# Optimization experiments

Hardware: AMD Instinct MI355X
Metric: run time of the kernel (lower is better)

The kernel has to match this reference:

```python
import jax, jax.numpy as jnp
import numpy as np

DIM = 512
HEADS = 8
DIM_HEAD = 64
INNER = HEADS * DIM_HEAD  # 512
EPS = 1e-5
SCALE = DIM_HEAD ** (-0.5)


def setup_inputs() -> dict:
    key = jax.random.key(0)
    ks = jax.random.split(key, 12)
    B, S = 8, 1024
    x = jax.random.normal(ks[0], (B, DIM, S, 1), dtype=jnp.float32)
    # BatchNorm2d params (eval mode: running stats)
    bn_gamma = jax.random.normal(ks[1], (DIM,), dtype=jnp.float32) * 0.1 + 1.0
    bn_beta = jax.random.normal(ks[2], (DIM,), dtype=jnp.float32) * 0.1
    bn_mean = jax.random.normal(ks[3], (DIM,), dtype=jnp.float32) * 0.1
    bn_var = jax.random.uniform(ks[4], (DIM,), dtype=jnp.float32, minval=0.5, maxval=1.5)
    # 1x1 Conv2d == linear: weight [out, in], bias [out]
    def lin(k, out_d, in_d):
        kw, kb = jax.random.split(k)
        lim = 1.0 / np.sqrt(in_d)
        w = jax.random.uniform(kw, (out_d, in_d), dtype=jnp.float32, minval=-lim, maxval=lim)
        b = jax.random.uniform(kb, (out_d,), dtype=jnp.float32, minval=-lim, maxval=lim)
        return w, b
    wq, bq = lin(ks[5], INNER, DIM)
    wk, bk = lin(ks[6], INNER, DIM)
    wv, bv = lin(ks[7], INNER, DIM)
    wo, bo = lin(ks[8], DIM, INNER)
    return {"x": x, "bn_gamma": bn_gamma, "bn_beta": bn_beta,
            "bn_mean": bn_mean, "bn_var": bn_var,
            "wq": wq, "bq": bq, "wk": wk, "bk": bk,
            "wv": wv, "bv": bv, "wo": wo, "bo": bo}


def reference(x, bn_gamma, bn_beta, bn_mean, bn_var,
              wq, bq, wk, bk, wv, bv, wo, bo):
    B, C, S, _ = x.shape
    # BatchNorm2d (eval) over channel dim
    inv = jax.lax.rsqrt(bn_var + EPS)
    xn = (x - bn_mean[None, :, None, None]) * (bn_gamma * inv)[None, :, None, None] \
         + bn_beta[None, :, None, None]
    t = jnp.transpose(xn[..., 0], (0, 2, 1))  # [B, S, C]
    q = (t @ wq.T + bq).reshape(B, S, HEADS, DIM_HEAD)
    k = (t @ wk.T + bk).reshape(B, S, HEADS, DIM_HEAD)
    v = (t @ wv.T + bv).reshape(B, S, HEADS, DIM_HEAD)
    scores = jnp.einsum('bshd,bthd->bhst', q, k) * SCALE  # [B,H,S,S]
    attn = jax.nn.softmax(scores, axis=-1)
    o = jnp.einsum('bhst,bthd->bshd', attn, v).reshape(B, S, INNER)
    y = o @ wo.T + bo  # [B, S, C]
    return jnp.transpose(y, (0, 2, 1))[..., None]  # [B, C, S, 1]
```

## Files before the change

kernel.cpp:

```cpp
#include <hip/hip_runtime.h>
#include <stdint.h>

typedef __bf16 bf16;
typedef bf16 bf16x8 __attribute__((ext_vector_type(8)));
typedef bf16 bf16x4 __attribute__((ext_vector_type(4)));
typedef float f32x4 __attribute__((ext_vector_type(4)));

#define NB 8
#define NS 1024
#define NC 512
#define NH 8
#define ND 64

#define QSCALE 0.18033688011f

__device__ __forceinline__ void gload16(const void* g, void* l) {
  __builtin_amdgcn_global_load_lds(
      (const __attribute__((address_space(1))) void*)g,
      (__attribute__((address_space(3))) void*)l, 16, 0, 0);
}

__global__ __launch_bounds__(256) void prep_kernel(
    const float* __restrict__ x, const float* __restrict__ gam,
    const float* __restrict__ bet, const float* __restrict__ mu,
    const float* __restrict__ var, const float* __restrict__ wq,
    const float* __restrict__ wk, const float* __restrict__ wv,
    const float* __restrict__ wo, bf16* __restrict__ t, bf16* __restrict__ wqb,
    bf16* __restrict__ wkb, bf16* __restrict__ wvb, bf16* __restrict__ wob) {
  __shared__ float tile[32][33];
  const int bid = blockIdx.x;
  if (bid < 4096) {
    const int b = bid >> 9, c0 = ((bid >> 5) & 15) << 5, s0 = (bid & 31) << 5;
    const int tx = threadIdx.x, sj = tx & 31, ci = tx >> 5;
#pragma unroll
    for (int kk = 0; kk < 4; ++kk) {
      const int c = c0 + ci + (kk << 3);
      const float sc = gam[c] * rsqrtf(var[c] + 1e-5f);
      const float sh = bet[c] - mu[c] * sc;
      tile[ci + (kk << 3)][sj] = x[(size_t)(b * NC + c) * NS + s0 + sj] * sc + sh;
    }
    __syncthreads();
#pragma unroll
    for (int kk = 0; kk < 4; ++kk) {
      const int s = s0 + ci + (kk << 3);
      t[(size_t)(b * NS + s) * NC + c0 + sj] = (bf16)tile[sj][ci + (kk << 3)];
    }
  } else {
    const int i = ((bid - 4096) * 256 + threadIdx.x) * 4;
    float4 a = *(const float4*)(&wq[i]);
    float4 b = *(const float4*)(&wk[i]);
    float4 c = *(const float4*)(&wv[i]);
    float4 d = *(const float4*)(&wo[i]);
    bf16x4 av = {(bf16)a.x, (bf16)a.y, (bf16)a.z, (bf16)a.w};
    bf16x4 bv = {(bf16)b.x, (bf16)b.y, (bf16)b.z, (bf16)b.w};
    bf16x4 cv = {(bf16)c.x, (bf16)c.y, (bf16)c.z, (bf16)c.w};
    bf16x4 dv = {(bf16)d.x, (bf16)d.y, (bf16)d.z, (bf16)d.w};
    *(bf16x4*)(&wqb[i]) = av;
    *(bf16x4*)(&wkb[i]) = bv;
    *(bf16x4*)(&wvb[i]) = cv;
    *(bf16x4*)(&wob[i]) = dv;
  }
}

__global__ __launch_bounds__(256) void gemm_qkv_kernel(
    const bf16* __restrict__ t, const bf16* __restrict__ wqb,
    const bf16* __restrict__ wkb, const bf16* __restrict__ wvb,
    const float* __restrict__ bq, const float* __restrict__ bk,
    const float* __restrict__ bv, bf16* __restrict__ qo, bf16* __restrict__ ko,
    bf16* __restrict__ vo) {
  __shared__ __align__(16) bf16 As[2][128 * 32];
  __shared__ __align__(16) bf16 Bs[2][128 * 32];
  const int lid = blockIdx.x;
  const int xcd = lid & 7, rr = lid >> 3;
  const int ny = rr % 12, mx = (rr / 12) * 8 + xcd;
  const int m0 = mx << 7, n0 = ny << 7;
  const int tid = threadIdx.x;
  const int wsel = n0 >> 9;
  const bf16* W = (wsel == 0) ? wqb : (wsel == 1 ? wkb : wvb);
  const float* bias = (wsel == 0) ? bq : (wsel == 1 ? bk : bv);
  const int nb = n0 & 511;
  const int w = tid >> 6, lane = tid & 63, l15 = lane & 15, l4 = lane >> 4;
  const int wm = (w >> 1) << 6, wn = (w & 1) << 6;

  const int srl = lane >> 2, sp = lane & 3;
  const int r0 = w * 16 + srl, r1 = 64 + w * 16 + srl;
  const int c0off = (sp ^ ((r0 >> 1) & 3)) << 3;
  const int c1off = (sp ^ ((r1 >> 1) & 3)) << 3;
  const bf16* a0 = t + (size_t)(m0 + r0) * 512 + c0off;
  const bf16* a1 = t + (size_t)(m0 + r1) * 512 + c1off;
  const bf16* b0 = W + (size_t)(nb + r0) * 512 + c0off;
  const bf16* b1 = W + (size_t)(nb + r1) * 512 + c1off;

  f32x4 acc[4][4] = {};
  gload16(a0, &As[0][w * 512]);
  gload16(a1, &As[0][2048 + w * 512]);
  gload16(b0, &Bs[0][w * 512]);
  gload16(b1, &Bs[0][2048 + w * 512]);
  __syncthreads();
  int buf = 0;
  for (int k0 = 0; k0 < 512; k0 += 32, buf ^= 1) {
    if (k0 + 32 < 512) {
      gload16(a0 + k0 + 32, &As[buf ^ 1][w * 512]);
      gload16(a1 + k0 + 32, &As[buf ^ 1][2048 + w * 512]);
      gload16(b0 + k0 + 32, &Bs[buf ^ 1][w * 512]);
      gload16(b1 + k0 + 32, &Bs[buf ^ 1][2048 + w * 512]);
    }
    bf16x8 af[4], bfv[4];
#pragma unroll
    for (int mi = 0; mi < 4; ++mi) {
      const int row = wm + mi * 16 + l15;
      af[mi] = *(const bf16x8*)(&As[buf][row * 32 + ((l4 ^ ((row >> 1) & 3)) << 3)]);
    }
#pragma unroll
    for (int ni = 0; ni < 4; ++ni) {
      const int row = wn + ni * 16 + l15;
      bfv[ni] = *(const bf16x8*)(&Bs[buf][row * 32 + ((l4 ^ ((row >> 1) & 3)) << 3)]);
    }
    if (wsel == 2) {
#pragma unroll
      for (int mi = 0; mi < 4; ++mi)
#pragma unroll
        for (int ni = 0; ni < 4; ++ni)
          acc[mi][ni] = __builtin_amdgcn_mfma_f32_16x16x32_bf16(
              af[mi], bfv[ni], acc[mi][ni], 0, 0, 0);
    } else {
#pragma unroll
      for (int mi = 0; mi < 4; ++mi)
#pragma unroll
        for (int ni = 0; ni < 4; ++ni)
          acc[mi][ni] = __builtin_amdgcn_mfma_f32_16x16x32_bf16(
              bfv[ni], af[mi], acc[mi][ni], 0, 0, 0);
    }
    __syncthreads();
  }
  const int bidx = m0 >> 10;
  if (wsel == 2) {
    const int sbase = (m0 & 1023) + wm + (l4 << 2);
#pragma unroll
    for (int ni = 0; ni < 4; ++ni) {
      const int nn = nb + wn + ni * 16 + l15;
      const int hh = nn >> 6, dd = nn & 63;
      const float bsv = bias[nn];
      bf16* vbase = vo + (size_t)(bidx * NH + hh) * (ND * NS) + (size_t)dd * NS + sbase;
#pragma unroll
      for (int mi = 0; mi < 4; ++mi) {
        bf16x4 pk;
#pragma unroll
        for (int r = 0; r < 4; ++r) pk[r] = (bf16)(acc[mi][ni][r] + bsv);
        *(bf16x4*)(&vbase[mi * 16]) = pk;
      }
    }
  } else {
    const bool isq = (wsel == 0);
    bf16* outp = isq ? qo : ko;
    const int sbase = (m0 & 1023) + wm + l15;
#pragma unroll
    for (int ni = 0; ni < 4; ++ni) {
      const int nn0 = nb + wn + ni * 16 + (l4 << 2);
      const int hh = nn0 >> 6, dd0 = nn0 & 63;
      const float4 bs4 = *(const float4*)(&bias[nn0]);
      bf16* obase = outp + (size_t)(bidx * NH + hh) * (NS * ND) + dd0;
#pragma unroll
      for (int mi = 0; mi < 4; ++mi) {
        bf16x4 pk;
        const float* bp = (const float*)&bs4;
#pragma unroll
        for (int r = 0; r < 4; ++r) {
          float val = acc[mi][ni][r] + bp[r];
          if (isq) val *= QSCALE;
          pk[r] = (bf16)val;
        }
        *(bf16x4*)(&obase[(size_t)(sbase + mi * 16) * ND]) = pk;
      }
    }
  }
}

__global__ __launch_bounds__(512, 4) void attn_kernel(
    const bf16* __restrict__ qg, const bf16* __restrict__ kg,
    const bf16* __restrict__ vtg, bf16* __restrict__ og) {
  __shared__ __align__(16) bf16 Kb[2][128 * 64];
  __shared__ __align__(16) bf16 Vb[2][64 * 128];
  __shared__ __align__(16) bf16 Ps[8][16 * 40];
  const int lid = blockIdx.x;
  const int xcd = lid & 7, rr = lid >> 3;
  const int bh = ((rr & 7) << 3) + xcd;
  const int q0 = (rr >> 3) << 7;
  const int tid = threadIdx.x, w = tid >> 6, lane = tid & 63;
  const int l15 = lane & 15, l4 = lane >> 4;
  const bf16* Qp = qg + ((size_t)bh * NS + q0) * ND;
  const bf16* Kp = kg + (size_t)bh * NS * ND;
  const bf16* Vp = vtg + (size_t)bh * ND * NS;

  bf16x8 qf[2];
#pragma unroll
  for (int kk = 0; kk < 2; ++kk)
    qf[kk] = *(const bf16x8*)(&Qp[(size_t)(w * 16 + l15) * ND + ((kk << 2) + l4) * 8]);

  const int krow = w * 16 + (lane >> 3);
  const bf16* ksrc = Kp + (size_t)krow * ND + (((lane & 7) ^ (krow & 7)) << 3);
  const int vrow1 = w * 8 + (lane >> 4);
  const int vrow2 = vrow1 + 4;
  const bf16* vsrc1 = Vp + (size_t)vrow1 * NS + (((lane & 15) ^ (vrow1 & 7)) << 3);
  const bf16* vsrc2 = Vp + (size_t)vrow2 * NS + (((lane & 15) ^ (vrow2 & 7)) << 3);

  f32x4 oacc[4] = {};
  float mrun = -1e30f, lrun = 0.f;

  gload16(ksrc, &Kb[0][w * 1024]);
  gload16(ksrc + 8 * ND, &Kb[0][w * 1024 + 512]);
  gload16(vsrc1, &Vb[0][w * 1024]);
  gload16(vsrc2, &Vb[0][w * 1024 + 512]);
  __syncthreads();

  int buf = 0;
  for (int kv0 = 0; kv0 < NS; kv0 += 128, buf ^= 1) {
    if (kv0 + 128 < NS) {
      gload16(ksrc + (size_t)(kv0 + 128) * ND, &Kb[buf ^ 1][w * 1024]);
      gload16(ksrc + (size_t)(kv0 + 136) * ND, &Kb[buf ^ 1][w * 1024 + 512]);
      gload16(vsrc1 + kv0 + 128, &Vb[buf ^ 1][w * 1024]);
      gload16(vsrc2 + kv0 + 128, &Vb[buf ^ 1][w * 1024 + 512]);
    }
    const bf16* Ks = Kb[buf];
    const bf16* Vs = Vb[buf];
    f32x4 st[8];
    __builtin_amdgcn_s_setprio(1);
#pragma unroll
    for (int rt = 0; rt < 8; ++rt) {
      const int row = rt * 16 + l15;
      const int rb = row * 64, s = row & 7;
      const bf16x8 a0 = *(const bf16x8*)(&Ks[rb + ((l4 ^ s) << 3)]);
      const bf16x8 a1 = *(const bf16x8*)(&Ks[rb + (((4 + l4) ^ s) << 3)]);
      f32x4 z = {0.f, 0.f, 0.f, 0.f};
      z = __builtin_amdgcn_mfma_f32_16x16x32_bf16(a0, qf[0], z, 0, 0, 0);
      st[rt] = __builtin_amdgcn_mfma_f32_16x16x32_bf16(a1, qf[1], z, 0, 0, 0);
    }
    __builtin_amdgcn_s_setprio(0);
    float pm = fmaxf(fmaxf(st[0][0], st[0][1]), fmaxf(st[0][2], st[0][3]));
#pragma unroll
    for (int rt = 1; rt < 8; ++rt)
      pm = fmaxf(pm, fmaxf(fmaxf(st[rt][0], st[rt][1]),
                           fmaxf(st[rt][2], st[rt][3])));
    pm = fmaxf(pm, __shfl_xor(pm, 16));
    pm = fmaxf(pm, __shfl_xor(pm, 32));
    if (!__all(pm - mrun <= 8.f)) {
      const float mnew = fmaxf(mrun, pm);
      const float alpha = __builtin_amdgcn_exp2f(mrun - mnew);
#pragma unroll
      for (int di = 0; di < 4; ++di)
#pragma unroll
        for (int r = 0; r < 4; ++r) oacc[di][r] *= alpha;
      lrun *= alpha;
      mrun = mnew;
    }
    float rs = 0.f;
    bf16* prow = &Ps[w][l15 * 40];
#pragma unroll
    for (int c = 0; c < 4; ++c) {
      bf16x4 pk1, pk2;
#pragma unroll
      for (int r = 0; r < 4; ++r) {
        const float p1 = __builtin_amdgcn_exp2f(st[2 * c][r] - mrun);
        const float p2 = __builtin_amdgcn_exp2f(st[2 * c + 1][r] - mrun);
        rs += p1 + p2;
        pk1[r] = (bf16)p1;
        pk2[r] = (bf16)p2;
      }
      *(bf16x4*)(&prow[4 * l4]) = pk1;
      *(bf16x4*)(&prow[16 + 4 * l4]) = pk2;
      const bf16x8 pa = *(const bf16x8*)(&prow[l4 * 8]);
      __builtin_amdgcn_s_setprio(1);
#pragma unroll
      for (int di = 0; di < 4; ++di) {
        const int vrow = di * 16 + l15;
        const int slot = (c << 2) + l4;
        const bf16x8 vf =
            *(const bf16x8*)(&Vs[vrow * 128 + ((slot ^ (vrow & 7)) << 3)]);
        oacc[di] = __builtin_amdgcn_mfma_f32_16x16x32_bf16(vf, pa, oacc[di], 0, 0, 0);
      }
      __builtin_amdgcn_s_setprio(0);
    }
    lrun += rs;
    __syncthreads();
  }
  lrun += __shfl_xor(lrun, 16);
  lrun += __shfl_xor(lrun, 32);
  const float linv = 1.f / lrun;
  const int b = bh >> 3, h = bh & 7;
  bf16* Op = og + (size_t)(b * NS + q0 + w * 16 + l15) * NC + h * ND + (l4 << 2);
#pragma unroll
  for (int di = 0; di < 4; ++di) {
    bf16x4 pk;
#pragma unroll
    for (int r = 0; r < 4; ++r) pk[r] = (bf16)(oacc[di][r] * linv);
    *(bf16x4*)(&Op[di * 16]) = pk;
  }
}

__global__ __launch_bounds__(256) void gemm_out_kernel(
    const bf16* __restrict__ wob, const bf16* __restrict__ o,
    const float* __restrict__ bo, float* __restrict__ out) {
  __shared__ __align__(16) bf16 As[2][64 * 32];
  __shared__ __align__(16) bf16 Bs[2][128 * 32];
  const int lid = blockIdx.x;
  const int xcd = lid & 7, rr = lid >> 3;
  const int mx = rr & 7, ny = ((rr >> 3) << 3) + xcd;
  const int m0 = mx << 6, n0 = ny << 7;
  const int tid = threadIdx.x;
  const int w = tid >> 6, lane = tid & 63, l15 = lane & 15, l4 = lane >> 4;
  const int wm = (w >> 1) << 5;
  const int wn = (w & 1) << 6;

  const int srl = lane >> 2, sp = lane & 3;
  const int ra = w * 16 + srl;
  const int caoff = (sp ^ ((ra >> 1) & 3)) << 3;
  const bf16* a0 = wob + (size_t)(m0 + ra) * 512 + caoff;
  const int rb0 = w * 16 + srl, rb1 = 64 + w * 16 + srl;
  const int cb0off = (sp ^ ((rb0 >> 1) & 3)) << 3;
  const int cb1off = (sp ^ ((rb1 >> 1) & 3)) << 3;
  const bf16* b0 = o + (size_t)(n0 + rb0) * 512 + cb0off;
  const bf16* b1 = o + (size_t)(n0 + rb1) * 512 + cb1off;

  f32x4 acc[2][4] = {};
  gload16(a0, &As[0][w * 512]);
  gload16(b0, &Bs[0][w * 512]);
  gload16(b1, &Bs[0][2048 + w * 512]);
  __syncthreads();
  int buf = 0;
  for (int k0 = 0; k0 < 512; k0 += 32, buf ^= 1) {
    if (k0 + 32 < 512) {
      gload16(a0 + k0 + 32, &As[buf ^ 1][w * 512]);
      gload16(b0 + k0 + 32, &Bs[buf ^ 1][w * 512]);
      gload16(b1 + k0 + 32, &Bs[buf ^ 1][2048 + w * 512]);
    }
    bf16x8 af[2], bfv[4];
#pragma unroll
    for (int mi = 0; mi < 2; ++mi) {
      const int row = wm + mi * 16 + l15;
      af[mi] = *(const bf16x8*)(&As[buf][row * 32 + ((l4 ^ ((row >> 1) & 3)) << 3)]);
    }
#pragma unroll
    for (int ni = 0; ni < 4; ++ni) {
      const int row = wn + ni * 16 + l15;
      bfv[ni] = *(const bf16x8*)(&Bs[buf][row * 32 + ((l4 ^ ((row >> 1) & 3)) << 3)]);
    }
#pragma unroll
    for (int mi = 0; mi < 2; ++mi)
#pragma unroll
      for (int ni = 0; ni < 4; ++ni)
        acc[mi][ni] = __builtin_amdgcn_mfma_f32_16x16x32_bf16(
            bfv[ni], af[mi], acc[mi][ni], 0, 0, 0);
    __syncthreads();
  }
  const int b = n0 >> 10;
  const int sb = (n0 & 1023) + wn;
#pragma unroll
  for (int mi = 0; mi < 2; ++mi) {
    const int cout = m0 + wm + mi * 16 + l15;
    const float bsv = bo[cout];
    float* obase = out + (size_t)(b * NC + cout) * NS;
#pragma unroll
    for (int ni = 0; ni < 4; ++ni) {
      const int s0i = sb + ni * 16 + (l4 << 2);
      float4 pk = {acc[mi][ni][0] + bsv, acc[mi][ni][1] + bsv,
                   acc[mi][ni][2] + bsv, acc[mi][ni][3] + bsv};
      *(float4*)(&obase[s0i]) = pk;
    }
  }
}

extern "C" void kernel_launch(void* const* d_in, const int* in_sizes, int n_in,
                              void* d_out, int out_size, void* d_ws,
                              size_t ws_size, hipStream_t stream) {
  const float* x = (const float*)d_in[0];
  const float* gam = (const float*)d_in[1];
  const float* bet = (const float*)d_in[2];
  const float* mu = (const float*)d_in[3];
  const float* var = (const float*)d_in[4];
  const float* wq = (const float*)d_in[5];
  const float* bq = (const float*)d_in[6];
  const float* wk = (const float*)d_in[7];
  const float* bk = (const float*)d_in[8];
  const float* wv = (const float*)d_in[9];
  const float* bv = (const float*)d_in[10];
  const float* wo = (const float*)d_in[11];
  const float* bo = (const float*)d_in[12];
  float* out = (float*)d_out;

  char* p = (char*)d_ws;
  const size_t big = (size_t)8192 * 512 * sizeof(bf16);
  bf16* t = (bf16*)p;   p += big;
  bf16* q = (bf16*)p;   p += big;
  bf16* k = (bf16*)p;   p += big;
  bf16* vt = (bf16*)p;  p += big;
  const size_t wsz = (size_t)512 * 512 * sizeof(bf16);
  bf16* wqb = (bf16*)p; p += wsz;
  bf16* wkb = (bf16*)p; p += wsz;
  bf16* wvb = (bf16*)p; p += wsz;
  bf16* wob = (bf16*)p; p += wsz;
  bf16* o = t;

  prep_kernel<<<dim3(4352), 256, 0, stream>>>(x, gam, bet, mu, var, wq, wk, wv,
                                              wo, t, wqb, wkb, wvb, wob);
  gemm_qkv_kernel<<<dim3(768), 256, 0, stream>>>(t, wqb, wkb, wvb, bq, bk, bv,
                                                 q, k, vt);
  attn_kernel<<<dim3(512), 512, 0, stream>>>(q, k, vt, o);
  gemm_out_kernel<<<dim3(512), 256, 0, stream>>>(wob, o, bo, out);
}
```

Measured before the change: 87.27 us.

## Rewrite attention with 32x32x16 MFMA and register-level P shuffle via permlane32_swap

The attention kernel moves from 16x16x32 MFMA tiles to 32x32x16 MFMA. Each wave now handles 32 query rows, a block has 4 waves, and the KV tile shrinks to 64. The softmax probabilities are repacked into the B-operand layout in registers with permlane32 swaps, which removes the LDS scratch round trip for P. The aim is fewer LDS accesses and fewer instructions per MFMA. In exchange there are more loop iterations with a barrier each, fewer threads per block, and higher register pressure from the 16-wide accumulators.

```diff
diff --git a/kernel.cpp b/kernel.cpp
--- a/kernel.cpp
+++ b/kernel.cpp
@@ -5,6 +5,7 @@
 typedef bf16 bf16x8 __attribute__((ext_vector_type(8)));
 typedef bf16 bf16x4 __attribute__((ext_vector_type(4)));
 typedef float f32x4 __attribute__((ext_vector_type(4)));
+typedef float f32x16 __attribute__((ext_vector_type(16)));
 
 #define NB 8
 #define NS 1024
@@ -18,6 +19,30 @@
   __builtin_amdgcn_global_load_lds(
       (const __attribute__((address_space(1))) void*)g,
       (__attribute__((address_space(3))) void*)l, 16, 0, 0);
+}
+
+__device__ __forceinline__ unsigned pk2(float lo, float hi) {
+  union { bf16 h[2]; unsigned u; } c;
+  c.h[0] = (bf16)lo;
+  c.h[1] = (bf16)hi;
+  return c.u;
+}
+
+__device__ __forceinline__ void plswap(unsigned& x, unsigned& y) {
+#if __has_builtin(__builtin_amdgcn_permlane32_swap)
+  typedef unsigned uint2v __attribute__((ext_vector_type(2)));
+  uint2v r = __builtin_amdgcn_permlane32_swap(x, y, false, false);
+  x = r[0];
+  y = r[1];
+#else
+  const bool hi = (threadIdx.x & 32) != 0;
+  const unsigned xs = (unsigned)__shfl_xor((int)x, 32);
+  const unsigned ys = (unsigned)__shfl_xor((int)y, 32);
+  const unsigned nx = hi ? ys : x;
+  const unsigned ny = hi ? y : xs;
+  x = nx;
+  y = ny;
+#endif
 }
 
 __global__ __launch_bounds__(256) void prep_kernel(
@@ -176,124 +201,128 @@
   }
 }
 
-__global__ __launch_bounds__(512, 4) void attn_kernel(
+__global__ __launch_bounds__(256, 2) void attn_kernel(
     const bf16* __restrict__ qg, const bf16* __restrict__ kg,
     const bf16* __restrict__ vtg, bf16* __restrict__ og) {
-  __shared__ __align__(16) bf16 Kb[2][128 * 64];
-  __shared__ __align__(16) bf16 Vb[2][64 * 128];
-  __shared__ __align__(16) bf16 Ps[8][16 * 40];
+  __shared__ __align__(16) bf16 Kb[2][64 * 64];
+  __shared__ __align__(16) bf16 Vb[2][64 * 64];
   const int lid = blockIdx.x;
   const int xcd = lid & 7, rr = lid >> 3;
   const int bh = ((rr & 7) << 3) + xcd;
   const int q0 = (rr >> 3) << 7;
   const int tid = threadIdx.x, w = tid >> 6, lane = tid & 63;
-  const int l15 = lane & 15, l4 = lane >> 4;
+  const int l31 = lane & 31, hi = lane >> 5;
   const bf16* Qp = qg + ((size_t)bh * NS + q0) * ND;
   const bf16* Kp = kg + (size_t)bh * NS * ND;
   const bf16* Vp = vtg + (size_t)bh * ND * NS;
 
-  bf16x8 qf[2];
-#pragma unroll
-  for (int kk = 0; kk < 2; ++kk)
-    qf[kk] = *(const bf16x8*)(&Qp[(size_t)(w * 16 + l15) * ND + ((kk << 2) + l4) * 8]);
-
-  const int krow = w * 16 + (lane >> 3);
-  const bf16* ksrc = Kp + (size_t)krow * ND + (((lane & 7) ^ (krow & 7)) << 3);
-  const int vrow1 = w * 8 + (lane >> 4);
-  const int vrow2 = vrow1 + 4;
-  const bf16* vsrc1 = Vp + (size_t)vrow1 * NS + (((lane & 15) ^ (vrow1 & 7)) << 3);
-  const bf16* vsrc2 = Vp + (size_t)vrow2 * NS + (((lane & 15) ^ (vrow2 & 7)) << 3);
-
-  f32x4 oacc[4] = {};
+  bf16x8 qf0, qf1, qf2, qf3;
+  {
+    const bf16* qrow = Qp + (size_t)(w * 32 + l31) * ND + hi * 8;
+    qf0 = *(const bf16x8*)(qrow);
+    qf1 = *(const bf16x8*)(qrow + 16);
+    qf2 = *(const bf16x8*)(qrow + 32);
+    qf3 = *(const bf16x8*)(qrow + 48);
+  }
+
+  const int srow = w * 16 + (lane >> 3);
+  const int sslot = (lane & 7) ^ (srow & 7);
+  const bf16* ksrc = Kp + (size_t)srow * ND + sslot * 8;
+  const bf16* vsrc = Vp + (size_t)srow * NS + sslot * 8;
+
+  f32x16 oacc0 = {}, oacc1 = {};
   float mrun = -1e30f, lrun = 0.f;
 
   gload16(ksrc, &Kb[0][w * 1024]);
   gload16(ksrc + 8 * ND, &Kb[0][w * 1024 + 512]);
-  gload16(vsrc1, &Vb[0][w * 1024]);
-  gload16(vsrc2, &Vb[0][w * 1024 + 512]);
+  gload16(vsrc, &Vb[0][w * 1024]);
+  gload16(vsrc + 8 * NS, &Vb[0][w * 1024 + 512]);
   __syncthreads();
 
+  const int s7 = l31 & 7;
   int buf = 0;
-  for (int kv0 = 0; kv0 < NS; kv0 += 128, buf ^= 1) {
-    if (kv0 + 128 < NS) {
-      gload16(ksrc + (size_t)(kv0 + 128) * ND, &Kb[buf ^ 1][w * 1024]);
-      gload16(ksrc + (size_t)(kv0 + 136) * ND, &Kb[buf ^ 1][w * 1024 + 512]);
-      gload16(vsrc1 + kv0 + 128, &Vb[buf ^ 1][w * 1024]);
-      gload16(vsrc2 + kv0 + 128, &Vb[buf ^ 1][w * 1024 + 512]);
+  for (int kv0 = 0; kv0 < NS; kv0 += 64, buf ^= 1) {
+    if (kv0 + 64 < NS) {
+      gload16(ksrc + (size_t)(kv0 + 64) * ND, &Kb[buf ^ 1][w * 1024]);
+      gload16(ksrc + (size_t)(kv0 + 72) * ND, &Kb[buf ^ 1][w * 1024 + 512]);
+      gload16(vsrc + kv0 + 64, &Vb[buf ^ 1][w * 1024]);
+      gload16(vsrc + 8 * NS + kv0 + 64, &Vb[buf ^ 1][w * 1024 + 512]);
     }
     const bf16* Ks = Kb[buf];
     const bf16* Vs = Vb[buf];
-    f32x4 st[8];
+    f32x16 st0 = {}, st1 = {};
     __builtin_amdgcn_s_setprio(1);
 #pragma unroll
-    for (int rt = 0; rt < 8; ++rt) {
-      const int row = rt * 16 + l15;
-      const int rb = row * 64, s = row & 7;
-      const bf16x8 a0 = *(const bf16x8*)(&Ks[rb + ((l4 ^ s) << 3)]);
-      const bf16x8 a1 = *(const bf16x8*)(&Ks[rb + (((4 + l4) ^ s) << 3)]);
-      f32x4 z = {0.f, 0.f, 0.f, 0.f};
-      z = __builtin_amdgcn_mfma_f32_16x16x32_bf16(a0, qf[0], z, 0, 0, 0);
-      st[rt] = __builtin_amdgcn_mfma_f32_16x16x32_bf16(a1, qf[1], z, 0, 0, 0);
+    for (int ks = 0; ks < 4; ++ks) {
+      const int sl = ((2 * ks + hi) ^ s7) << 3;
+      const bf16x8 a0 = *(const bf16x8*)(&Ks[l31 * 64 + sl]);
+      const bf16x8 a1 = *(const bf16x8*)(&Ks[(32 + l31) * 64 + sl]);
+      const bf16x8 qk = (ks == 0) ? qf0 : (ks == 1) ? qf1 : (ks == 2) ? qf2 : qf3;
+      st0 = __builtin_amdgcn_mfma_f32_32x32x16_bf16(a0, qk, st0, 0, 0, 0);
+      st1 = __builtin_amdgcn_mfma_f32_32x32x16_bf16(a1, qk, st1, 0, 0, 0);
     }
     __builtin_amdgcn_s_setprio(0);
-    float pm = fmaxf(fmaxf(st[0][0], st[0][1]), fmaxf(st[0][2], st[0][3]));
-#pragma unroll
-    for (int rt = 1; rt < 8; ++rt)
-      pm = fmaxf(pm, fmaxf(fmaxf(st[rt][0], st[rt][1]),
-                           fmaxf(st[rt][2], st[rt][3])));
-    pm = fmaxf(pm, __shfl_xor(pm, 16));
+    float pm = st0[0];
+#pragma unroll
+    for (int i = 1; i < 16; ++i) pm = fmaxf(pm, st0[i]);
+#pragma unroll
+    for (int i = 0; i < 16; ++i) pm = fmaxf(pm, st1[i]);
     pm = fmaxf(pm, __shfl_xor(pm, 32));
     if (!__all(pm - mrun <= 8.f)) {
       const float mnew = fmaxf(mrun, pm);
       const float alpha = __builtin_amdgcn_exp2f(mrun - mnew);
 #pragma unroll
-      for (int di = 0; di < 4; ++di)
-#pragma unroll
-        for (int r = 0; r < 4; ++r) oacc[di][r] *= alpha;
+      for (int i = 0; i < 16; ++i) {
+        oacc0[i] *= alpha;
+        oacc1[i] *= alpha;
+      }
       lrun *= alpha;
       mrun = mnew;
     }
     float rs = 0.f;
-    bf16* prow = &Ps[w][l15 * 40];
-#pragma unroll
-    for (int c = 0; c < 4; ++c) {
-      bf16x4 pk1, pk2;
-#pragma unroll
-      for (int r = 0; r < 4; ++r) {
-        const float p1 = __builtin_amdgcn_exp2f(st[2 * c][r] - mrun);
-        const float p2 = __builtin_amdgcn_exp2f(st[2 * c + 1][r] - mrun);
-        rs += p1 + p2;
-        pk1[r] = (bf16)p1;
-        pk2[r] = (bf16)p2;
+#pragma unroll
+    for (int t = 0; t < 4; ++t) {
+      float p[8];
+#pragma unroll
+      for (int i = 0; i < 8; ++i) {
+        const float sv = (t < 2) ? st0[8 * (t & 1) + i] : st1[8 * (t & 1) + i];
+        p[i] = __builtin_amdgcn_exp2f(sv - mrun);
+        rs += p[i];
       }
-      *(bf16x4*)(&prow[4 * l4]) = pk1;
-      *(bf16x4*)(&prow[16 + 4 * l4]) = pk2;
-      const bf16x8 pa = *(const bf16x8*)(&prow[l4 * 8]);
+      unsigned c01 = pk2(p[0], p[1]), c23 = pk2(p[2], p[3]);
+      unsigned c45 = pk2(p[4], p[5]), c67 = pk2(p[6], p[7]);
+      plswap(c01, c45);
+      plswap(c23, c67);
+      union { unsigned u[4]; bf16x8 v; } pu;
+      pu.u[0] = c01;
+      pu.u[1] = c23;
+      pu.u[2] = c45;
+      pu.u[3] = c67;
+      const int sl = ((2 * t + hi) ^ s7) << 3;
+      const bf16x8 v0 = *(const bf16x8*)(&Vs[l31 * 64 + sl]);
+      const bf16x8 v1 = *(const bf16x8*)(&Vs[(32 + l31) * 64 + sl]);
       __builtin_amdgcn_s_setprio(1);
-#pragma unroll
-      for (int di = 0; di < 4; ++di) {
-        const int vrow = di * 16 + l15;
-        const int slot = (c << 2) + l4;
-        const bf16x8 vf =
-            *(const bf16x8*)(&Vs[vrow * 128 + ((slot ^ (vrow & 7)) << 3)]);
-        oacc[di] = __builtin_amdgcn_mfma_f32_16x16x32_bf16(vf, pa, oacc[di], 0, 0, 0);
-      }
+      oacc0 = __builtin_amdgcn_mfma_f32_32x32x16_bf16(v0, pu.v, oacc0, 0, 0, 0);
+      oacc1 = __builtin_amdgcn_mfma_f32_32x32x16_bf16(v1, pu.v, oacc1, 0, 0, 0);
       __builtin_amdgcn_s_setprio(0);
     }
     lrun += rs;
     __syncthreads();
   }
-  lrun += __shfl_xor(lrun, 16);
   lrun += __shfl_xor(lrun, 32);
   const float linv = 1.f / lrun;
   const int b = bh >> 3, h = bh & 7;
-  bf16* Op = og + (size_t)(b * NS + q0 + w * 16 + l15) * NC + h * ND + (l4 << 2);
-#pragma unroll
-  for (int di = 0; di < 4; ++di) {
-    bf16x4 pk;
-#pragma unroll
-    for (int r = 0; r < 4; ++r) pk[r] = (bf16)(oacc[di][r] * linv);
-    *(bf16x4*)(&Op[di * 16]) = pk;
+  bf16* Op = og + (size_t)(b * NS + q0 + w * 32 + l31) * NC + h * ND;
+#pragma unroll
+  for (int g = 0; g < 4; ++g) {
+    bf16x4 pk0, pk1;
+#pragma unroll
+    for (int r = 0; r < 4; ++r) {
+      pk0[r] = (bf16)(oacc0[4 * g + r] * linv);
+      pk1[r] = (bf16)(oacc1[4 * g + r] * linv);
+    }
+    *(bf16x4*)(&Op[g * 8 + 4 * hi]) = pk0;
+    *(bf16x4*)(&Op[32 + g * 8 + 4 * hi]) = pk1;
   }
 }
 
@@ -404,6 +433,6 @@
                                               wo, t, wqb, wkb, wvb, wob);
   gemm_qkv_kernel<<<dim3(768), 256, 0, stream>>>(t, wqb, wkb, wvb, bq, bk, bv,
                                                  q, k, vt);
-  attn_kernel<<<dim3(512), 512, 0, stream>>>(q, k, vt, o);
+  attn_kernel<<<dim3(512), 256, 0, stream>>>(q, k, vt, o);
   gemm_out_kernel<<<dim3(512), 256, 0, stream>>>(wob, o, bo, out);
 }
```

Result: no change. 86.43 us (-1.0%).
